# Optimization experiments

Measured on AMD Instinct MI355X. Metric: run time of the kernel, lower is better.

Reference implementation:

```python
import jax, jax.numpy as jnp
import numpy as np

R = 3          # radius
T_STEPS = 2    # T
F = 200        # fingerprint_dim
AOUT = 39
BOUT = 10
B, L, N, NB = 128, 256, 8, 512


def _gru(x, h, wih, whh, bih, bhh):
    # PyTorch GRUCell semantics; wih/whh: [3F, F], gate order r,z,n
    gi = x @ wih.T + bih
    gh = h @ whh.T + bhh
    ir, iz, inn = jnp.split(gi, 3, axis=-1)
    hr, hz, hn = jnp.split(gh, 3, axis=-1)
    r = jax.nn.sigmoid(ir + hr)
    z = jax.nn.sigmoid(iz + hz)
    n = jnp.tanh(inn + r * hn)
    return (1.0 - z) * n + z * h


def _seg_softmax(x, lo, hi):
    idx = jnp.arange(x.shape[-1])
    m = ((idx >= lo) & (idx < hi)).astype(x.dtype)
    s = jax.nn.softmax(x + (1.0 - m) * (-9e8), axis=-1)
    return s * m


def _unit_act(x, i, fn):
    m = (jnp.arange(x.shape[-1]) == i).astype(x.dtype)
    return fn(x * m) * m


def setup_inputs() -> dict:
    key = jax.random.key(0)
    ks = jax.random.split(key, 24)
    rn = lambda k, s, sc=0.05: (jax.random.normal(k, s, jnp.float32) * sc)
    inp = {
        'atom_list': rn(ks[0], (B, L, AOUT), 1.0),
        'bond_list': rn(ks[1], (B, NB, BOUT), 1.0),
        'atom_degree_list': jax.random.randint(ks[2], (B, L, N), 0, L),
        'bond_degree_list': jax.random.randint(ks[3], (B, L, N), 0, NB),
        'atom_mask': jnp.ones((B, L), jnp.float32),
        'mol_feature': rn(ks[4], (B, F), 1.0),
        'activated_features': jax.nn.relu(rn(ks[5], (B, L, F), 1.0)),
        # params
        'atom_fc_w': rn(ks[6], (AOUT, F)), 'atom_fc_b': jnp.zeros((AOUT,), jnp.float32),
        'bond_fc_w': rn(ks[7], (BOUT, 2 * F)), 'bond_fc_b': jnp.zeros((BOUT,), jnp.float32),
        'align_w': rn(ks[8], (R, F, 2 * F)), 'align_b': jnp.zeros((R, F), jnp.float32),
        'attend_w': rn(ks[9], (R, F, F)), 'attend_b': jnp.zeros((R, F), jnp.float32),
        'gru_wih': rn(ks[10], (R, 3 * F, F)), 'gru_whh': rn(ks[11], (R, 3 * F, F)),
        'gru_bih': jnp.zeros((R, 3 * F), jnp.float32), 'gru_bhh': jnp.zeros((R, 3 * F), jnp.float32),
        'mol_align_w': rn(ks[12], (F, 2 * F)), 'mol_align_b': jnp.zeros((F,), jnp.float32),
        'mol_gru_wih': rn(ks[13], (3 * F, F)), 'mol_gru_whh': rn(ks[14], (3 * F, F)),
        'mol_gru_bih': jnp.zeros((3 * F,), jnp.float32), 'mol_gru_bhh': jnp.zeros((3 * F,), jnp.float32),
    }
    return inp


def reference(atom_list, bond_list, atom_degree_list, bond_degree_list, atom_mask,
              mol_feature, activated_features,
              atom_fc_w, atom_fc_b, bond_fc_w, bond_fc_b,
              align_w, align_b, attend_w, attend_b,
              gru_wih, gru_whh, gru_bih, gru_bhh,
              mol_align_w, mol_align_b,
              mol_gru_wih, mol_gru_whh, mol_gru_bih, mol_gru_bhh):
    f32 = jnp.float32
    b, l, _ = atom_list.shape
    fdim = mol_feature.shape[-1]
    gather = jax.vmap(lambda feats, idx: feats[idx])  # [L,F],[L,N] -> [L,N,F]

    pad = (atom_degree_list == l - 1)
    attend_mask = jnp.where(pad, 0.0, 1.0).astype(f32)[..., None]      # [B,L,N,1]
    softmax_mask = jnp.where(pad, -9e8, 0.0).astype(f32)[..., None]    # [B,L,N,1]

    # molecular feature -> per-atom git feature (T GRU steps)
    mol_exp = jnp.broadcast_to(mol_feature[:, None, :], (b, l, fdim))
    mw = jax.nn.softmax(jnp.sum(mol_exp * activated_features, axis=-1), axis=-1)  # [B,L]
    git = mw[..., None] * mol_exp + activated_features
    for _t in range(T_STEPS):
        ctx = jax.nn.elu(jnp.concatenate([mol_exp, git], axis=-1) @ mol_align_w.T + mol_align_b)
        git = _gru(ctx.reshape(b * l, fdim), git.reshape(b * l, fdim),
                   mol_gru_wih, mol_gru_whh, mol_gru_bih, mol_gru_bhh).reshape(b, l, fdim)
        act = jax.nn.relu(git)

    # radius-1 rounds of neighbor attention + GRU update
    for d in range(R - 1):
        nbr = gather(act, atom_degree_list)                             # [B,L,N,F]
        exp = jnp.broadcast_to(act[:, :, None, :], nbr.shape)
        feat_align = jnp.concatenate([exp, nbr], axis=-1)               # [B,L,N,2F]
        score = jax.nn.leaky_relu(feat_align @ align_w[d].T + align_b[d], 0.01)
        score = score + softmax_mask
        attw = jax.nn.softmax(score, axis=-2) * attend_mask             # [B,L,N,F]
        nt = nbr @ attend_w[d].T + attend_b[d]
        context = jax.nn.elu(jnp.sum(attw * nt, axis=-2))               # [B,L,F]
        h = _gru(context.reshape(b * l, fdim), act.reshape(b * l, fdim),
                 gru_wih[d], gru_whh[d], gru_bih[d], gru_bhh[d])
        act = jax.nn.relu(h.reshape(b, l, fdim))

    # decode atoms and bonds
    al = act @ atom_fc_w.T + atom_fc_b                                  # [B,L,AOUT]
    nbr = gather(act, atom_degree_list)                                 # [B,L,N,F]
    exp = jnp.broadcast_to(act[:, :, None, :], nbr.shape)
    bl = jnp.concatenate([exp, nbr], axis=-1) @ bond_fc_w.T + bond_fc_b  # [B,L,N,BOUT]

    sig = jax.nn.sigmoid
    activate_atom = (_seg_softmax(al, 0, 16) + _seg_softmax(al, 16, 22)
                     + _seg_softmax(al, 24, 30) + _seg_softmax(al, 31, 36)
                     + _unit_act(al, 24, jax.nn.relu)
                     + _unit_act(al, 30, sig) + _unit_act(al, 36, sig)
                     + _unit_act(al, 37, sig) + _unit_act(al, 38, sig))
    activate_bond = (_seg_softmax(bl, 0, 4) + _seg_softmax(bl, 6, 10)
                     + _unit_act(bl, 4, sig) + _unit_act(bl, 5, sig))
    return (activate_atom, activate_bond)
```

## Files before the change

kernel.cpp:

```cpp
#include <hip/hip_runtime.h>
#include <hip/hip_bf16.h>

#define FDIM 200
#define BB   128
#define LL   256
#define NN   8
#define BL   (BB*LL)
#define AOUTD 39
#define BOUTD 10
#define KCH  28

#define P0 0
#define P1 17920
#define P2 25088
#define P3 43008
#define P4 78848
#define P5 96768
#define P6 132608
#define P7 150528
#define WCHUNKS 154112
#define NBIAS 4864

typedef short v8s __attribute__((ext_vector_type(8)));
typedef float v4f __attribute__((ext_vector_type(4)));

__device__ __forceinline__ float bf2f(unsigned short u){
  union { unsigned int i; float f; } v; v.i = ((unsigned int)u) << 16; return v.f;
}
__device__ __forceinline__ unsigned short f2bf(float f){
  unsigned int x = __float_as_uint(f);
  x += 0x7fffu + ((x >> 16) & 1u);
  return (unsigned short)(x >> 16);
}
__device__ __forceinline__ float ldf(const void* p, long long i, bool bf){
  return bf ? bf2f(((const unsigned short*)p)[i]) : ((const float*)p)[i];
}
__device__ __forceinline__ void stf(void* p, size_t i, float v, bool bf){
  if (bf) ((unsigned short*)p)[i] = f2bf(v);
  else    ((float*)p)[i] = v;
}
__device__ __forceinline__ float bflo(unsigned int q){
  union { unsigned int i; float f; } v; v.i = q << 16; return v.f;
}
__device__ __forceinline__ float bfhi(unsigned int q){
  union { unsigned int i; float f; } v; v.i = q & 0xffff0000u; return v.f;
}
__device__ __forceinline__ void ld8(const unsigned short* p, float* o){
  uint4 q = *(const uint4*)p;
  o[0]=bflo(q.x); o[1]=bfhi(q.x); o[2]=bflo(q.y); o[3]=bfhi(q.y);
  o[4]=bflo(q.z); o[5]=bfhi(q.z); o[6]=bflo(q.w); o[7]=bfhi(q.w);
}
__device__ __forceinline__ void ld8g(const void* p, size_t i, bool bf, float* o){
  if (bf){ ld8((const unsigned short*)p + i, o); }
  else {
    const float4* q = (const float4*)((const float*)p + i);
    float4 x = q[0], y = q[1];
    o[0]=x.x; o[1]=x.y; o[2]=x.z; o[3]=x.w;
    o[4]=y.x; o[5]=y.y; o[6]=y.z; o[7]=y.w;
  }
}
__device__ __forceinline__ void st8(unsigned short* p, const float* v){
  uint4 q;
  q.x = (unsigned int)f2bf(v[0]) | ((unsigned int)f2bf(v[1]) << 16);
  q.y = (unsigned int)f2bf(v[2]) | ((unsigned int)f2bf(v[3]) << 16);
  q.z = (unsigned int)f2bf(v[4]) | ((unsigned int)f2bf(v[5]) << 16);
  q.w = (unsigned int)f2bf(v[6]) | ((unsigned int)f2bf(v[7]) << 16);
  *(uint4*)p = q;
}
__device__ __forceinline__ float dotF(const void* wp, size_t off, const float* x, bool bf){
  float a0=0.f,a1=0.f,a2=0.f,a3=0.f;
  if (bf){
    const uint4* p = (const uint4*)((const unsigned short*)wp + off);
#pragma unroll
    for (int c = 0; c < FDIM/8; ++c){
      uint4 q = p[c];
      const float* xb = x + c*8;
      a0 += bflo(q.x)*xb[0]; a1 += bfhi(q.x)*xb[1];
      a2 += bflo(q.y)*xb[2]; a3 += bfhi(q.y)*xb[3];
      a0 += bflo(q.z)*xb[4]; a1 += bfhi(q.z)*xb[5];
      a2 += bflo(q.w)*xb[6]; a3 += bfhi(q.w)*xb[7];
    }
  } else {
    const float4* p = (const float4*)((const float*)wp + off);
#pragma unroll
    for (int c = 0; c < FDIM/4; ++c){
      float4 q = p[c];
      const float* xb = x + c*4;
      a0 += q.x*xb[0]; a1 += q.y*xb[1]; a2 += q.z*xb[2]; a3 += q.w*xb[3];
    }
  }
  return (a0+a1)+(a2+a3);
}
__device__ __forceinline__ float sigm(float x){ return 1.f/(1.f+__expf(-x)); }
__device__ __forceinline__ float tanh_(float x){
  float cx = fminf(fmaxf(x, -15.f), 15.f);
  float e = __expf(2.f*cx);
  return (e - 1.f)/(e + 1.f);
}
__device__ __forceinline__ float elu_(float x){ return x > 0.f ? x : __expf(x) - 1.f; }

__global__ void k_probe(const unsigned int* __restrict__ amask, int* __restrict__ mode){
  if (blockIdx.x == 0 && threadIdx.x == 0)
    *mode = (amask[0] == 0x3F803F80u) ? 1 : 0;
}

__global__ __launch_bounds__(256) void k_repack(unsigned short* __restrict__ wrep,
    const void* mwhh, const void* maw, const void* mwih,
    const void* alw, const void* atw, const void* gwhh, const void* gwih,
    const void* afw, const void* bfw, const int* __restrict__ mode){
  const bool bf = (*mode != 0);
  int idx = blockIdx.x*256 + threadIdx.x;
  if (idx >= WCHUNKS) return;
  int pb, Ng;
  if (idx < P1)      { pb = P0; Ng = 640;  }
  else if (idx < P2) { pb = P1; Ng = 256;  }
  else if (idx < P3) { pb = P2; Ng = 640;  }
  else if (idx < P4) { pb = P3; Ng = 1280; }
  else if (idx < P5) { pb = P4; Ng = 640;  }
  else if (idx < P6) { pb = P5; Ng = 1280; }
  else if (idx < P7) { pb = P6; Ng = 640;  }
  else               { pb = P7; Ng = 128;  }
  int li = idx - pb;
  int c = li / Ng, n = li - c*Ng;
  const void* S = nullptr; long long sb = 0; int rl = 0, off = 0, row = 0, N = 0;
  if (pb == P0)      { S = mwhh; rl = 200; row = n; N = 600; }
  else if (pb == P1) { S = maw;  rl = 400; off = 200; row = n; N = 200; }
  else if (pb == P2) { S = mwih; rl = 200; row = n; N = 600; }
  else if (pb == P3 || pb == P5){
    long long d = (pb == P5) ? 1 : 0; N = 1200;
    if (n < 200)      { S = alw;  sb = d*80000;  rl = 400; off = 0;   row = n; }
    else if (n < 400) { S = alw;  sb = d*80000;  rl = 400; off = 200; row = n-200; }
    else if (n < 600) { S = atw;  sb = d*40000;  rl = 200; off = 0;   row = n-400; }
    else              { S = gwhh; sb = d*120000; rl = 200; off = 0;   row = n-600; }
  }
  else if (pb == P4 || pb == P6){
    long long d = (pb == P6) ? 1 : 0;
    S = gwih; sb = d*120000; rl = 200; row = n; N = 600;
  } else {
    N = 64;
    if (n < 39)                { S = afw; rl = 200; row = n; }
    else if (n >= 40 && n < 50){ S = bfw; rl = 400; off = 0;   row = n-40; }
    else if (n >= 50 && n < 60){ S = bfw; rl = 400; off = 200; row = n-50; }
  }
  float v[8];
#pragma unroll
  for (int j = 0; j < 8; j++){
    int k = c*8 + j;
    v[j] = (S && n < N && k < 200) ? ldf(S, sb + (long long)row*rl + off + k, bf) : 0.f;
  }
  st8(wrep + (size_t)idx*8, v);
}

__global__ __launch_bounds__(256) void k_biases(float* __restrict__ bt,
    const void* mbhh, const void* mbih, const void* alb, const void* atb,
    const void* gbhh, const void* gbih, const void* afb, const void* bfb,
    const int* __restrict__ mode){
  const bool bf = (*mode != 0);
  int e = blockIdx.x*256 + threadIdx.x;
  if (e >= NBIAS) return;
  float v = 0.f;
  if (e < 600)        v = ldf(mbhh, e, bf);
  else if (e < 1200)  v = ldf(mbih, e-600, bf);
  else if (e < 4800){
    int q = e - 1200; int d = q / 1800; q -= d*1800;
    if (q < 1200){
      if (q < 200)      v = ldf(alb, (long long)d*200 + q, bf);
      else if (q < 400) v = 0.f;
      else if (q < 600) v = ldf(atb, (long long)d*200 + q-400, bf);
      else              v = ldf(gbhh, (long long)d*600 + q-600, bf);
    } else              v = ldf(gbih, (long long)d*600 + q-1200, bf);
  } else {
    int q = e - 4800;
    if (q < 39)                 v = ldf(afb, q, bf);
    else if (q >= 40 && q < 50) v = ldf(bfb, q-40, bf);
  }
  bt[e] = v;
}

__global__ __launch_bounds__(256, 5) void k_gemm(
    const unsigned short* __restrict__ A,
    const unsigned short* __restrict__ Wc, int wNg, int npan,
    unsigned short* __restrict__ C, int ldc, int Nout,
    int emode, const float* __restrict__ bias, int gbase)
{
  __shared__ unsigned short Ws[KCH*64*8];
  int t = threadIdx.x;
  int bid = blockIdx.x;
  int res = bid & 7, q = bid >> 3;
  int p = q % npan;
  int mt = (q / npan)*8 + res;
  int nbase = p * 64;
  int mbase = mt * 128;
  const uint4* Wg = (const uint4*)Wc;
  uint4* Wl = (uint4*)Ws;
  for (int i = t; i < KCH*64; i += 256){
    int c = i >> 6, n = i & 63;
    Wl[i] = Wg[(size_t)c*wNg + nbase + n];
  }
  __syncthreads();
  int wave = t >> 6, lane = t & 63;
  int quad = lane >> 4, l16 = lane & 15;
  const unsigned short* A0 = A + (size_t)(mbase + wave*32 + l16)*FDIM + quad*8;
  v4f acc[2][4];
#pragma unroll
  for (int ms = 0; ms < 2; ms++)
#pragma unroll
    for (int ns = 0; ns < 4; ns++) acc[ms][ns] = (v4f){0.f,0.f,0.f,0.f};
#pragma unroll
  for (int ks = 0; ks < 7; ks++){
    v8s a0 = *(const v8s*)(A0 + ks*32);
    v8s a1 = *(const v8s*)(A0 + 16*FDIM + ks*32);
    const unsigned short* Bp = Ws + ((ks*4 + quad)*64 + l16)*8;
#pragma unroll
    for (int ns = 0; ns < 4; ns++){
      v8s b = *(const v8s*)(Bp + ns*128);
      acc[0][ns] = __builtin_amdgcn_mfma_f32_16x16x32_bf16(a0, b, acc[0][ns], 0, 0, 0);
      acc[1][ns] = __builtin_amdgcn_mfma_f32_16x16x32_bf16(a1, b, acc[1][ns], 0, 0, 0);
    }
  }
  int colb = nbase + l16;
  int rowb = mbase + wave*32 + quad*4;
  const float* pr = (emode == 2) ? (bias + (size_t)(((gbase + mbase) >> 8))*FDIM) : nullptr;
#pragma unroll
  for (int ms = 0; ms < 2; ms++){
#pragma unroll
    for (int ns = 0; ns < 4; ns++){
      int col = colb + ns*16;
      if (col < Nout){
        float badd = (emode == 1) ? bias[col] : 0.f;
        float pv   = (emode == 2) ? pr[col] : 0.f;
        unsigned short* Cp = C + (size_t)(rowb + ms*16)*ldc + col;
#pragma unroll
        for (int reg = 0; reg < 4; reg++){
          float v = acc[ms][ns][reg] + badd;
          if (emode == 2) v = elu_(pv + v);
          Cp[(size_t)reg*ldc] = f2bf(v);
        }
      }
    }
  }
}

__global__ __launch_bounds__(256) void k_premol(float* __restrict__ pre,
    const void* __restrict__ molf, const void* __restrict__ maw,
    const void* __restrict__ mab, const int* __restrict__ mode){
  const bool bf = (*mode != 0);
  int b = blockIdx.x, t = threadIdx.x;
  __shared__ float mf[FDIM];
  for (int f = t; f < FDIM; f += 256) mf[f] = ldf(molf, (size_t)b*FDIM+f, bf);
  __syncthreads();
  for (int f = t; f < FDIM; f += 256)
    pre[b*FDIM+f] = ldf(mab, f, bf) + dotF(maw, (size_t)f*2*FDIM, mf, bf);
}

__global__ __launch_bounds__(LL) void k_gitdot(float* __restrict__ mw_out,
    const void* __restrict__ molf, const void* __restrict__ actf,
    const int* __restrict__ mode){
  const bool bf = (*mode != 0);
  int b = blockIdx.x, l = threadIdx.x;
  __shared__ float mf[FDIM];
  __shared__ float red[LL];
  for (int f = l; f < FDIM; f += LL) mf[f] = ldf(molf, (size_t)b*FDIM+f, bf);
  __syncthreads();
  float d = dotF(actf, ((size_t)b*LL + l)*FDIM, mf, bf);
  red[l] = d; __syncthreads();
  for (int s = 128; s > 0; s >>= 1){ if (l < s) red[l] = fmaxf(red[l], red[l+s]); __syncthreads(); }
  float m = red[0]; __syncthreads();
  float e = __expf(d - m);
  red[l] = e; __syncthreads();
  for (int s = 128; s > 0; s >>= 1){ if (l < s) red[l] += red[l+s]; __syncthreads(); }
  mw_out[(size_t)b*LL + l] = e / red[0];
}

__global__ __launch_bounds__(256) void k_gitwrite(unsigned short* __restrict__ act,
    const void* __restrict__ molf, const void* __restrict__ actf,
    const float* __restrict__ mw, const int* __restrict__ mode){
  const bool bf = (*mode != 0);
  int idx = blockIdx.x*256 + threadIdx.x;
  if (idx >= BL*25) return;
  int row = idx/25, f0 = (idx - row*25)*8;
  int b = row >> 8;
  float m = mw[row];
  float mv[8], av[8], v[8];
  ld8g(molf, (size_t)b*FDIM + f0, bf, mv);
  ld8g(actf, (size_t)row*FDIM + f0, bf, av);
#pragma unroll
  for (int j = 0; j < 8; j++) v[j] = m*mv[j] + av[j];
  st8(act + (size_t)row*FDIM + f0, v);
}

__global__ __launch_bounds__(256) void k_gru_ew(unsigned short* __restrict__ act,
    const unsigned short* __restrict__ big, int gio, int gho,
    int dorelu, int total){
  int idx = blockIdx.x*256 + threadIdx.x;
  if (idx >= total) return;
  int row = idx/25, f0 = (idx - row*25)*8;
  size_t g = (size_t)row*1200;
  float gr[8], gz[8], gn[8], hr[8], hz[8], hn_[8], h[8], o[8];
  ld8(big + g + gio + f0,       gr);
  ld8(big + g + gio + 200 + f0, gz);
  ld8(big + g + gio + 400 + f0, gn);
  ld8(big + g + gho + f0,       hr);
  ld8(big + g + gho + 200 + f0, hz);
  ld8(big + g + gho + 400 + f0, hn_);
  ld8(act + (size_t)row*FDIM + f0, h);
#pragma unroll
  for (int j = 0; j < 8; j++){
    float r = sigm(gr[j] + hr[j]);
    float z = sigm(gz[j] + hz[j]);
    float n = tanh_(gn[j] + r*hn_[j]);
    float hn = (1.f - z)*n + z*h[j];
    o[j] = dorelu ? fmaxf(hn, 0.f) : hn;
  }
  st8(act + (size_t)row*FDIM + f0, o);
}

__global__ __launch_bounds__(256) void k_attn_ew(const unsigned short* __restrict__ big,
    unsigned short* __restrict__ ctx, const int* __restrict__ adeg,
    int base, int total){
  int idx = blockIdx.x*256 + threadIdx.x;
  if (idx >= total) return;
  int a = idx/25, f0 = (idx - a*25)*8;
  int mb = (a >> 8) << 8;
  float s0[8];
  ld8(big + (size_t)a*1200 + f0, s0);
  int4 d0 = *(const int4*)(adeg + (size_t)(base + a)*NN);
  int4 d1 = *(const int4*)(adeg + (size_t)(base + a)*NN + 4);
  int iv[NN] = {d0.x, d0.y, d0.z, d0.w, d1.x, d1.y, d1.z, d1.w};
  int nid[NN]; float nmul[NN], nadd[NN];
#pragma unroll
  for (int n = 0; n < NN; n++){
    nid[n] = mb + iv[n];
    bool pad = (iv[n] == LL-1);
    nmul[n] = pad ? 0.f : 1.f;
    nadd[n] = pad ? -9e8f : 0.f;
  }
  float e[NN][8], mx[8];
#pragma unroll
  for (int j = 0; j < 8; j++) mx[j] = -1e30f;
#pragma unroll
  for (int n = 0; n < NN; n++){
    float p[8];
    ld8(big + (size_t)nid[n]*1200 + 200 + f0, p);
#pragma unroll
    for (int j = 0; j < 8; j++){
      float s = s0[j] + p[j];
      s = s > 0.f ? s : 0.01f*s;
      s += nadd[n];
      e[n][j] = s;
      mx[j] = fmaxf(mx[j], s);
    }
  }
  float sum[8] = {0,0,0,0,0,0,0,0};
#pragma unroll
  for (int n = 0; n < NN; n++)
#pragma unroll
    for (int j = 0; j < 8; j++){ e[n][j] = __expf(e[n][j] - mx[j]); sum[j] += e[n][j]; }
  float acc[8] = {0,0,0,0,0,0,0,0};
#pragma unroll
  for (int n = 0; n < NN; n++){
    float q[8];
    ld8(big + (size_t)nid[n]*1200 + 400 + f0, q);
#pragma unroll
    for (int j = 0; j < 8; j++) acc[j] += e[n][j]*nmul[n]*q[j];
  }
  float o[8];
#pragma unroll
  for (int j = 0; j < 8; j++) o[j] = elu_(acc[j]/sum[j]);
  st8(ctx + (size_t)a*FDIM + f0, o);
}

__global__ __launch_bounds__(256) void k_dec(const unsigned short* __restrict__ big,
    const int* __restrict__ adeg, void* __restrict__ out, int base,
    const int* __restrict__ mode){
  const bool bf = (*mode != 0);
  const size_t obase = (size_t)BL*AOUTD;
  int sub = threadIdx.x >> 6, tl = threadIdx.x & 63;
  int a = blockIdx.x*4 + sub;
  __shared__ float al[4][40];
  __shared__ float sm[4][4], ss[4][4];
  const int lo[4] = {0,16,24,31}, hi[4] = {16,22,30,36};
  if (tl < AOUTD) al[sub][tl] = bf2f(big[(size_t)a*64 + tl]);
  __syncthreads();
  if (tl < 4){
    float m = -1e30f;
    for (int k = lo[tl]; k < hi[tl]; k++) m = fmaxf(m, al[sub][k]);
    float s = 0.f;
    for (int k = lo[tl]; k < hi[tl]; k++) s += __expf(al[sub][k]-m);
    sm[sub][tl] = m; ss[sub][tl] = s;
  }
  __syncthreads();
  if (tl < AOUTD){
    float v = 0.f;
#pragma unroll
    for (int g = 0; g < 4; g++)
      if (tl >= lo[g] && tl < hi[g]) v += __expf(al[sub][tl]-sm[sub][g])/ss[sub][g];
    if (tl == 24) v += fmaxf(al[sub][24], 0.f);
    if (tl == 30 || tl == 36 || tl == 37 || tl == 38) v += sigm(al[sub][tl]);
    stf(out, (size_t)(base + a)*AOUTD + tl, v, bf);
  } else if (tl >= 40 && tl < 48){
    int n = tl - 40;
    int iv = adeg[((size_t)(base + a))*NN + n];
    int vr = ((a >> 8) << 8) + iv;
    float bl[BOUTD];
#pragma unroll
    for (int o = 0; o < BOUTD; o++)
      bl[o] = bf2f(big[(size_t)a*64 + 40 + o]) + bf2f(big[(size_t)vr*64 + 50 + o]);
    float v[BOUTD];
    float m0 = fmaxf(fmaxf(bl[0],bl[1]), fmaxf(bl[2],bl[3]));
    float e0[4], s0 = 0.f;
#pragma unroll
    for (int j = 0; j < 4; j++){ e0[j] = __expf(bl[j]-m0); s0 += e0[j]; }
    float m1 = fmaxf(fmaxf(bl[6],bl[7]), fmaxf(bl[8],bl[9]));
    float e1[4], s1 = 0.f;
#pragma unroll
    for (int j = 0; j < 4; j++){ e1[j] = __expf(bl[6+j]-m1); s1 += e1[j]; }
#pragma unroll
    for (int j = 0; j < 4; j++) v[j] = e0[j]/s0;
    v[4] = sigm(bl[4]); v[5] = sigm(bl[5]);
#pragma unroll
    for (int j = 0; j < 4; j++) v[6+j] = e1[j]/s1;
    size_t op = obase + ((size_t)(base + a)*NN + n)*BOUTD;
#pragma unroll
    for (int j = 0; j < BOUTD; j++) stf(out, op + j, v[j], bf);
  }
}

extern "C" void kernel_launch(void* const* d_in, const int* in_sizes, int n_in,
                              void* d_out, int out_size, void* d_ws, size_t ws_size,
                              hipStream_t stream) {
  const int* adeg = (const int*)d_in[2];
  const void* amask = d_in[4];
  const void* molf = d_in[5];
  const void* actf = d_in[6];
  const void* afw = d_in[7];  const void* afb = d_in[8];
  const void* bfw = d_in[9];  const void* bfb = d_in[10];
  const void* alw = d_in[11]; const void* alb = d_in[12];
  const void* atw = d_in[13]; const void* atb = d_in[14];
  const void* gwih = d_in[15]; const void* gwhh = d_in[16];
  const void* gbih = d_in[17]; const void* gbhh = d_in[18];
  const void* maw = d_in[19]; const void* mab = d_in[20];
  const void* mwih = d_in[21]; const void* mwhh = d_in[22];
  const void* mbih = d_in[23]; const void* mbhh = d_in[24];

  char* w = (char*)d_ws;
  unsigned short* act  = (unsigned short*)w;  w += (size_t)BL*FDIM*2;
  float*          mw   = (float*)w;           w += (size_t)BL*4;
  float*          pre  = (float*)w;           w += (size_t)BB*FDIM*4;
  unsigned short* wrep = (unsigned short*)w;  w += (size_t)WCHUNKS*16;
  float*          bt   = (float*)w;           w += (size_t)NBIAS*4;
  int*            mode = (int*)w;             w += 16;
  size_t fixed = (size_t)(w - (char*)d_ws);
  int CH = 8192;
  if (ws_size >= fixed + (size_t)32768*2800) CH = 32768;
  else if (ws_size >= fixed + (size_t)16384*2800) CH = 16384;
  unsigned short* ctx = (unsigned short*)w;   w += (size_t)CH*FDIM*2;
  unsigned short* big = (unsigned short*)w;
  const int NCH = BL / CH;
  const int EWT = CH*25, EWB = EWT/256;
  const int GY = CH/128;

  k_probe<<<1, 64, 0, stream>>>((const unsigned int*)amask, mode);
  k_repack<<<(WCHUNKS + 255)/256, 256, 0, stream>>>(wrep, mwhh, maw, mwih,
      alw, atw, gwhh, gwih, afw, bfw, mode);
  k_biases<<<(NBIAS + 255)/256, 256, 0, stream>>>(bt, mbhh, mbih, alb, atb,
      gbhh, gbih, afb, bfb, mode);
  k_premol<<<BB, 256, 0, stream>>>(pre, molf, maw, mab, mode);
  k_gitdot<<<BB, LL, 0, stream>>>(mw, molf, actf, mode);
  k_gitwrite<<<(BL*25 + 255)/256, 256, 0, stream>>>(act, molf, actf, mw, mode);

  for (int ts = 0; ts < 2; ts++){
    for (int c = 0; c < NCH; c++){
      int base = c*CH;
      unsigned short* Ac = act + (size_t)base*FDIM;
      k_gemm<<<10*GY, 256, 0, stream>>>(Ac, wrep + (size_t)P0*8, 640, 10,
          big, 1200, 600, 1, bt + 0, 0);
      k_gemm<<<4*GY, 256, 0, stream>>>(Ac, wrep + (size_t)P1*8, 256, 4,
          ctx, FDIM, FDIM, 2, pre, base);
      k_gemm<<<10*GY, 256, 0, stream>>>(ctx, wrep + (size_t)P2*8, 640, 10,
          big + 600, 1200, 600, 1, bt + 600, 0);
      k_gru_ew<<<EWB, 256, 0, stream>>>(Ac, big, 600, 0, (ts==1), EWT);
    }
  }
  for (int d = 0; d < 2; d++){
    size_t pA = (d ? P5 : P3), pB = (d ? P6 : P4);
    float* btA = bt + 1200 + d*1800;
    float* btB = bt + 2400 + d*1800;
    for (int c = 0; c < NCH; c++){
      int base = c*CH;
      unsigned short* Ac = act + (size_t)base*FDIM;
      k_gemm<<<19*GY, 256, 0, stream>>>(Ac, wrep + pA*8, 1280, 19,
          big, 1200, 1200, 1, btA, 0);
      k_attn_ew<<<EWB, 256, 0, stream>>>(big, ctx, adeg, base, EWT);
      k_gemm<<<10*GY, 256, 0, stream>>>(ctx, wrep + pB*8, 640, 10,
          big, 1200, 600, 1, btB, 0);
      k_gru_ew<<<EWB, 256, 0, stream>>>(Ac, big, 0, 600, 1, EWT);
    }
  }
  for (int c = 0; c < NCH; c++){
    int base = c*CH;
    unsigned short* Ac = act + (size_t)base*FDIM;
    k_gemm<<<1*GY, 256, 0, stream>>>(Ac, wrep + (size_t)P7*8, 128, 1,
        big, 64, 64, 1, bt + 4800, 0);
    k_dec<<<CH/4, 256, 0, stream>>>(big, adeg, d_out, base, mode);
  }
}
```

Before: 605.4 us.

## Fuse GRU input-gate GEMM with GRU elementwise update into one kernel

Adds a fused kernel that computes the x@W_ih GEMM for all three gates of a 64-feature slice and applies the GRU cell update directly in the epilogue, writing the new hidden state. The W_ih weights are repacked with each gate padded to 256 columns so one block can load the r, z and n slices together. This removes the separate gate GEMM output write to the big buffer and the standalone elementwise GRU kernel, along with their launches and global round trips. In exchange the block holds three times the accumulators, which raises register pressure, and the epilogue does scattered bf16 loads of the hidden-side gates.

```diff
diff --git a/kernel.cpp b/kernel.cpp
--- a/kernel.cpp
+++ b/kernel.cpp
@@ -13,12 +13,12 @@
 #define P0 0
 #define P1 17920
 #define P2 25088
-#define P3 43008
-#define P4 78848
-#define P5 96768
-#define P6 132608
-#define P7 150528
-#define WCHUNKS 154112
+#define P3 46592
+#define P4 82432
+#define P5 103936
+#define P6 139776
+#define P7 161280
+#define WCHUNKS 164864
 #define NBIAS 4864
 
 typedef short v8s __attribute__((ext_vector_type(8)));
@@ -111,31 +111,34 @@
   const bool bf = (*mode != 0);
   int idx = blockIdx.x*256 + threadIdx.x;
   if (idx >= WCHUNKS) return;
-  int pb, Ng;
+  int pb, Ng, pad = 0; long long d = 0;
   if (idx < P1)      { pb = P0; Ng = 640;  }
   else if (idx < P2) { pb = P1; Ng = 256;  }
-  else if (idx < P3) { pb = P2; Ng = 640;  }
+  else if (idx < P3) { pb = P2; Ng = 768;  pad = 1; }
   else if (idx < P4) { pb = P3; Ng = 1280; }
-  else if (idx < P5) { pb = P4; Ng = 640;  }
-  else if (idx < P6) { pb = P5; Ng = 1280; }
-  else if (idx < P7) { pb = P6; Ng = 640;  }
+  else if (idx < P5) { pb = P4; Ng = 768;  pad = 1; }
+  else if (idx < P6) { pb = P5; Ng = 1280; d = 1; }
+  else if (idx < P7) { pb = P6; Ng = 768;  pad = 1; d = 1; }
   else               { pb = P7; Ng = 128;  }
   int li = idx - pb;
   int c = li / Ng, n = li - c*Ng;
   const void* S = nullptr; long long sb = 0; int rl = 0, off = 0, row = 0, N = 0;
-  if (pb == P0)      { S = mwhh; rl = 200; row = n; N = 600; }
+  if (pad){
+    int gate = n >> 8, f = n & 255;
+    if (f < 200){
+      S = (pb == P2) ? mwih : gwih;
+      sb = (pb == P2) ? 0 : d*120000;
+      rl = 200; off = 0; row = gate*200 + f; N = Ng;
+    }
+  }
+  else if (pb == P0)      { S = mwhh; rl = 200; row = n; N = 600; }
   else if (pb == P1) { S = maw;  rl = 400; off = 200; row = n; N = 200; }
-  else if (pb == P2) { S = mwih; rl = 200; row = n; N = 600; }
   else if (pb == P3 || pb == P5){
-    long long d = (pb == P5) ? 1 : 0; N = 1200;
+    N = 1200;
     if (n < 200)      { S = alw;  sb = d*80000;  rl = 400; off = 0;   row = n; }
     else if (n < 400) { S = alw;  sb = d*80000;  rl = 400; off = 200; row = n-200; }
     else if (n < 600) { S = atw;  sb = d*40000;  rl = 200; off = 0;   row = n-400; }
     else              { S = gwhh; sb = d*120000; rl = 200; off = 0;   row = n-600; }
-  }
-  else if (pb == P4 || pb == P6){
-    long long d = (pb == P6) ? 1 : 0;
-    S = gwih; sb = d*120000; rl = 200; row = n; N = 600;
   } else {
     N = 64;
     if (n < 39)                { S = afw; rl = 200; row = n; }
@@ -241,6 +244,81 @@
   }
 }
 
+__global__ __launch_bounds__(256, 3) void k_gemm_gru(
+    const unsigned short* __restrict__ ctxA,
+    const unsigned short* __restrict__ Wc,
+    unsigned short* __restrict__ act,
+    const unsigned short* __restrict__ big, int gho,
+    const float* __restrict__ gib, int dorelu)
+{
+  __shared__ unsigned short Ws[3*KCH*64*8];
+  int t = threadIdx.x, bid = blockIdx.x;
+  int res = bid & 7, q = bid >> 3;
+  int p = q & 3;
+  int mt = (q >> 2)*8 + res;
+  int f0 = p*64;
+  int mbase = mt*128;
+  const uint4* Wg = (const uint4*)Wc;
+  uint4* Wl = (uint4*)Ws;
+  for (int i = t; i < 3*KCH*64; i += 256){
+    int g = i / (KCH*64), r2 = i - g*(KCH*64);
+    int c = r2 >> 6, n = r2 & 63;
+    Wl[i] = Wg[(size_t)c*768 + g*256 + f0 + n];
+  }
+  __syncthreads();
+  int wave = t >> 6, lane = t & 63;
+  int quad = lane >> 4, l16 = lane & 15;
+  const unsigned short* A0 = ctxA + (size_t)(mbase + wave*32 + l16)*FDIM + quad*8;
+  v4f acc[3][2][4];
+#pragma unroll
+  for (int g = 0; g < 3; g++)
+#pragma unroll
+    for (int ms = 0; ms < 2; ms++)
+#pragma unroll
+      for (int ns = 0; ns < 4; ns++) acc[g][ms][ns] = (v4f){0.f,0.f,0.f,0.f};
+#pragma unroll
+  for (int ks = 0; ks < 7; ks++){
+    v8s a0 = *(const v8s*)(A0 + ks*32);
+    v8s a1 = *(const v8s*)(A0 + 16*FDIM + ks*32);
+#pragma unroll
+    for (int g = 0; g < 3; g++){
+      const unsigned short* Bp = Ws + ((size_t)(g*KCH + ks*4 + quad)*64 + l16)*8;
+#pragma unroll
+      for (int ns = 0; ns < 4; ns++){
+        v8s b = *(const v8s*)(Bp + ns*128);
+        acc[g][0][ns] = __builtin_amdgcn_mfma_f32_16x16x32_bf16(a0, b, acc[g][0][ns], 0, 0, 0);
+        acc[g][1][ns] = __builtin_amdgcn_mfma_f32_16x16x32_bf16(a1, b, acc[g][1][ns], 0, 0, 0);
+      }
+    }
+  }
+  int rowb = mbase + wave*32 + quad*4;
+#pragma unroll
+  for (int ms = 0; ms < 2; ms++){
+#pragma unroll
+    for (int ns = 0; ns < 4; ns++){
+      int f = f0 + ns*16 + l16;
+      if (f < 200){
+        float br = gib[f], bz = gib[200+f], bn = gib[400+f];
+#pragma unroll
+        for (int reg = 0; reg < 4; reg++){
+          int row = rowb + ms*16 + reg;
+          size_t gb = (size_t)row*1200 + gho;
+          float ghr = bf2f(big[gb + f]);
+          float ghz = bf2f(big[gb + 200 + f]);
+          float ghn = bf2f(big[gb + 400 + f]);
+          float h = bf2f(act[(size_t)row*FDIM + f]);
+          float r = sigm(acc[0][ms][ns][reg] + br + ghr);
+          float z = sigm(acc[1][ms][ns][reg] + bz + ghz);
+          float n = tanh_(acc[2][ms][ns][reg] + bn + r*ghn);
+          float hn = (1.f - z)*n + z*h;
+          if (dorelu) hn = fmaxf(hn, 0.f);
+          act[(size_t)row*FDIM + f] = f2bf(hn);
+        }
+      }
+    }
+  }
+}
+
 __global__ __launch_bounds__(256) void k_premol(float* __restrict__ pre,
     const void* __restrict__ molf, const void* __restrict__ maw,
     const void* __restrict__ mab, const int* __restrict__ mode){
@@ -287,32 +365,6 @@
 #pragma unroll
   for (int j = 0; j < 8; j++) v[j] = m*mv[j] + av[j];
   st8(act + (size_t)row*FDIM + f0, v);
-}
-
-__global__ __launch_bounds__(256) void k_gru_ew(unsigned short* __restrict__ act,
-    const unsigned short* __restrict__ big, int gio, int gho,
-    int dorelu, int total){
-  int idx = blockIdx.x*256 + threadIdx.x;
-  if (idx >= total) return;
-  int row = idx/25, f0 = (idx - row*25)*8;
-  size_t g = (size_t)row*1200;
-  float gr[8], gz[8], gn[8], hr[8], hz[8], hn_[8], h[8], o[8];
-  ld8(big + g + gio + f0,       gr);
-  ld8(big + g + gio + 200 + f0, gz);
-  ld8(big + g + gio + 400 + f0, gn);
-  ld8(big + g + gho + f0,       hr);
-  ld8(big + g + gho + 200 + f0, hz);
-  ld8(big + g + gho + 400 + f0, hn_);
-  ld8(act + (size_t)row*FDIM + f0, h);
-#pragma unroll
-  for (int j = 0; j < 8; j++){
-    float r = sigm(gr[j] + hr[j]);
-    float z = sigm(gz[j] + hz[j]);
-    float n = tanh_(gn[j] + r*hn_[j]);
-    float hn = (1.f - z)*n + z*h[j];
-    o[j] = dorelu ? fmaxf(hn, 0.f) : hn;
-  }
-  st8(act + (size_t)row*FDIM + f0, o);
 }
 
 __global__ __launch_bounds__(256) void k_attn_ew(const unsigned short* __restrict__ big,
@@ -477,24 +529,22 @@
           big, 1200, 600, 1, bt + 0, 0);
       k_gemm<<<4*GY, 256, 0, stream>>>(Ac, wrep + (size_t)P1*8, 256, 4,
           ctx, FDIM, FDIM, 2, pre, base);
-      k_gemm<<<10*GY, 256, 0, stream>>>(ctx, wrep + (size_t)P2*8, 640, 10,
-          big + 600, 1200, 600, 1, bt + 600, 0);
-      k_gru_ew<<<EWB, 256, 0, stream>>>(Ac, big, 600, 0, (ts==1), EWT);
+      k_gemm_gru<<<4*GY, 256, 0, stream>>>(ctx, wrep + (size_t)P2*8,
+          Ac, big, 0, bt + 600, (ts==1));
     }
   }
   for (int d = 0; d < 2; d++){
     size_t pA = (d ? P5 : P3), pB = (d ? P6 : P4);
     float* btA = bt + 1200 + d*1800;
-    float* btB = bt + 2400 + d*1800;
+    float* gib = bt + 2400 + d*1800;
     for (int c = 0; c < NCH; c++){
       int base = c*CH;
       unsigned short* Ac = act + (size_t)base*FDIM;
       k_gemm<<<19*GY, 256, 0, stream>>>(Ac, wrep + pA*8, 1280, 19,
           big, 1200, 1200, 1, btA, 0);
       k_attn_ew<<<EWB, 256, 0, stream>>>(big, ctx, adeg, base, EWT);
-      k_gemm<<<10*GY, 256, 0, stream>>>(ctx, wrep + pB*8, 640, 10,
-          big, 1200, 600, 1, btB, 0);
-      k_gru_ew<<<EWB, 256, 0, stream>>>(Ac, big, 0, 600, 1, EWT);
+      k_gemm_gru<<<4*GY, 256, 0, stream>>>(ctx, wrep + pB*8,
+          Ac, big, 600, gib, 1);
     }
   }
   for (int c = 0; c < NCH; c++){
```

Measured after the change: 648.1 us. +7.1%, slower.
